# Kernel tuning notes

Hardware: AMD Instinct MI355X
Metric: run time of the kernel (lower is better)

Reference implementation:

```python
import jax, jax.numpy as jnp
import numpy as np

E, H, M, IN, T = 4, 64, 64, 32, 32      # e_size, hidden_state, message, in_size, target
HL = (128, 256, 128)                     # NNet hidden layers (priba's NNet default)
N_LAYERS = 3


def setup_inputs() -> dict:
    key = jax.random.key(0)
    ks = iter(jax.random.split(key, 64))
    B, N = 16, 128

    def w(shape, scale=0.1):
        return jax.random.normal(next(ks), shape, dtype=jnp.float32) * scale

    inp = {
        "h_in": jax.random.normal(next(ks), (B, N, IN), dtype=jnp.float32),
        "am": jax.random.normal(next(ks), (B, N, N, E), dtype=jnp.float32),
        "g_size": jax.random.randint(next(ks), (B,), 0, N),
    }
    # EdgeNetwork NNet: E -> 128 -> 256 -> 128 -> M*H
    dims_e = (E,) + HL + (M * H,)
    for i in range(4):
        inp[f"We{i}"] = w((dims_e[i], dims_e[i + 1]))
        inp[f"be{i}"] = w((dims_e[i + 1],))
    # GRU (torch nn.GRU, one layer, one step): input M, hidden H
    inp["Wih"] = w((3 * H, M)); inp["Whh"] = w((3 * H, H))
    inp["bih"] = w((3 * H,)); inp["bhh"] = w((3 * H,))
    # Readout NNets: i on [h_T, h_0] (H+IN -> T), j on h_T (H -> T)
    dims_i = (H + IN,) + HL + (T,)
    dims_j = (H,) + HL + (T,)
    for i in range(4):
        inp[f"Wi{i}"] = w((dims_i[i], dims_i[i + 1])); inp[f"bi{i}"] = w((dims_i[i + 1],))
        inp[f"Wj{i}"] = w((dims_j[i], dims_j[i + 1])); inp[f"bj{i}"] = w((dims_j[i + 1],))
    return inp


def _mlp(x, Ws, bs):
    for Wk, bk in zip(Ws[:-1], bs[:-1]):
        x = jax.nn.relu(x @ Wk + bk)
    return x @ Ws[-1] + bs[-1]


def reference(h_in, am, g_size,
              We0, be0, We1, be1, We2, be2, We3, be3,
              Wih, Whh, bih, bhh,
              Wi0, bi0, Wi1, bi1, Wi2, bi2, Wi3, bi3,
              Wj0, bj0, Wj1, bj1, Wj2, bj2, Wj3, bj3):
    B, N, _ = h_in.shape
    h = jnp.pad(h_in, ((0, 0), (0, 0), (0, H - IN)))            # pad to hidden size
    mask = (jnp.arange(N)[None, :] < g_size[:, None]).astype(h.dtype)[:, :, None]  # [B,N,1]

    # Edge-network hidden features; final linear layer is fused into the
    # message contraction to avoid materializing per-edge [M,H] matrices.
    f = am                                                       # [B,N,N,E]
    for Wk, bk in ((We0, be0), (We1, be1), (We2, be2)):
        f = jax.nn.relu(f @ Wk + bk)                             # [B,N,N,128]
    W3 = We3.reshape(HL[-1], M, H)                               # [128,M,H]
    b3 = be3.reshape(M, H)

    for _ in range(N_LAYERS):                                    # weight-tied GGNN steps
        # m[b,v,o] = sum_w (A(e_bvw) @ h_bw)[o], A = reshape(f @ We3 + be3)
        t = jnp.einsum('bvwk,bwi->bvki', f, h)                   # [B,N,128,H]
        msg = jnp.einsum('bvki,koi->bvo', t, W3)
        msg = msg + jnp.einsum('oi,bi->bo', b3, h.sum(1))[:, None, :]
        # single-step torch GRU update
        gi = msg @ Wih.T + bih
        gh = h @ Whh.T + bhh
        r = jax.nn.sigmoid(gi[..., :H] + gh[..., :H])
        z = jax.nn.sigmoid(gi[..., H:2 * H] + gh[..., H:2 * H])
        n = jnp.tanh(gi[..., 2 * H:] + r * gh[..., 2 * H:])
        h = (1.0 - z) * n + z * h
        h = h * mask

    # GGNN readout: sum_v mask * sigmoid(i([h_T, h_0])) * j(h_T), then log_softmax
    gate = jax.nn.sigmoid(_mlp(jnp.concatenate([h, h_in], -1),
                               (Wi0, Wi1, Wi2, Wi3), (bi0, bi1, bi2, bi3)))
    val = _mlp(h, (Wj0, Wj1, Wj2, Wj3), (bj0, bj1, bj2, bj3))
    res = (mask * gate * val).sum(1)                             # [B,T]
    return jax.nn.log_softmax(res, axis=1)
```

## Files before the change

kernel.cpp:

```cpp
#include <hip/hip_runtime.h>
#include <math.h>

#define B   16
#define N   128
#define E   4
#define H   64
#define M   64
#define IN_ 32
#define T   32
#define K1  128
#define K2  256
#define K3  128

typedef _Float16 f16;
typedef f16  f16x8 __attribute__((ext_vector_type(8)));
typedef f16  f16x4 __attribute__((ext_vector_type(4)));
typedef f16  f16x2 __attribute__((ext_vector_type(2)));
typedef float f32x4 __attribute__((ext_vector_type(4)));

#define MFMA16(a, b, c) __builtin_amdgcn_mfma_f32_16x16x32_f16(a, b, c, 0, 0, 0)

#define OFF_W1T   0
#define OFF_W2T   32768
#define OFF_WE3H  65536
#define OFF_RI0   589824
#define OFF_RI1   602112
#define OFF_RI2   634880
#define OFF_RI3   667648
#define OFF_RJ0   671744
#define OFF_RJ1   679936
#define OFF_RJ2   712704
#define OFF_RJ3   745472
#define WPACK_SZ  749568

union SmemU {
    struct { float xl[64][4]; f16 y1[64][136]; f16 y2[64][264]; } e;
    union {
        struct { f16 Al[128][72]; f16 Bl[128][72]; } in;
        f16 Ol[128][136];
    } pg;
    struct { float prt[8][64]; float hsum[64]; float bias[64]; } bi;
};

__global__ __launch_bounds__(256) void prep_kernel(
    const float* __restrict__ h_in,
    const float* __restrict__ We1, const float* __restrict__ We2,
    const float* __restrict__ We3,
    const float* __restrict__ Wi0, const float* __restrict__ Wi1,
    const float* __restrict__ Wi2, const float* __restrict__ Wi3,
    const float* __restrict__ Wj0, const float* __restrict__ Wj1,
    const float* __restrict__ Wj2, const float* __restrict__ Wj3,
    float* __restrict__ h, f16* __restrict__ h16, f16* __restrict__ hin16,
    f16* __restrict__ wp) {
    int idx = blockIdx.x * 256 + threadIdx.x;
    if (idx < B * N * H) {
        int i  = idx & (H - 1);
        int bn = idx >> 6;
        float v = (i < IN_) ? h_in[bn * IN_ + i] : 0.f;
        h[idx] = v;
        h16[idx] = (f16)v;
        if (i < IN_) hin16[bn * IN_ + i] = (f16)v;
    }
    if (idx >= WPACK_SZ) return;
    if (idx < OFF_W2T) {
        int j = idx >> 7, k = idx & 127;
        wp[idx] = (f16)We1[k * 256 + j];
    } else if (idx < OFF_WE3H) {
        int t = idx - OFF_W2T;
        int j = t >> 8, k = t & 255;
        wp[idx] = (f16)We2[k * 128 + j];
    } else if (idx < OFF_RI0) {
        wp[idx] = (f16)We3[idx - OFF_WE3H];
    } else if (idx < OFF_RI1) {
        int t = idx - OFF_RI0;
        int n = t / 96, c = t % 96;
        wp[idx] = (f16)Wi0[c * 128 + n];
    } else if (idx < OFF_RI2) {
        int t = idx - OFF_RI1;
        int n = t >> 7, k = t & 127;
        wp[idx] = (f16)Wi1[k * 256 + n];
    } else if (idx < OFF_RI3) {
        int t = idx - OFF_RI2;
        int n = t >> 8, k = t & 255;
        wp[idx] = (f16)Wi2[k * 128 + n];
    } else if (idx < OFF_RJ0) {
        int t = idx - OFF_RI3;
        int n = t >> 7, k = t & 127;
        wp[idx] = (f16)Wi3[k * 32 + n];
    } else if (idx < OFF_RJ1) {
        int t = idx - OFF_RJ0;
        int n = t >> 6, c = t & 63;
        wp[idx] = (f16)Wj0[c * 128 + n];
    } else if (idx < OFF_RJ2) {
        int t = idx - OFF_RJ1;
        int n = t >> 7, k = t & 127;
        wp[idx] = (f16)Wj1[k * 256 + n];
    } else if (idx < OFF_RJ3) {
        int t = idx - OFF_RJ2;
        int n = t >> 8, k = t & 255;
        wp[idx] = (f16)Wj2[k * 128 + n];
    } else {
        int t = idx - OFF_RJ3;
        int n = t >> 7, k = t & 127;
        wp[idx] = (f16)Wj3[k * 32 + n];
    }
}


__device__ void edge_body(SmemU& su, int tid, int tile,
                          const float* __restrict__ am,
                          const float* __restrict__ We0,
                          const float* __restrict__ be0,
                          const f16* __restrict__ W1t,
                          const float* __restrict__ be1,
                          const f16* __restrict__ W2t,
                          const float* __restrict__ be2,
                          f16* __restrict__ f) {
    int lane = tid & 63, wv = tid >> 6;
    long long g0 = (long long)tile * 64;

    if (tid < 256) ((float*)su.e.xl)[tid] = am[g0 * 4 + tid];
    __syncthreads();

    {
        int j0 = (tid & 63) * 2, e0 = (tid >> 6) * 8;
        float w00 = We0[j0],       w01 = We0[j0 + 1];
        float w10 = We0[128 + j0], w11 = We0[128 + j0 + 1];
        float w20 = We0[256 + j0], w21 = We0[256 + j0 + 1];
        float w30 = We0[384 + j0], w31 = We0[384 + j0 + 1];
        float b0 = be0[j0], b1 = be0[j0 + 1];
        #pragma unroll 4
        for (int e = e0; e < e0 + 8; ++e) {
            float x0 = su.e.xl[e][0], x1 = su.e.xl[e][1];
            float x2 = su.e.xl[e][2], x3 = su.e.xl[e][3];
            float v0 = b0 + x0 * w00 + x1 * w10 + x2 * w20 + x3 * w30;
            float v1 = b1 + x0 * w01 + x1 * w11 + x2 * w21 + x3 * w31;
            f16x2 p;
            p[0] = (f16)fmaxf(v0, 0.f);
            p[1] = (f16)fmaxf(v1, 0.f);
            *(f16x2*)&su.e.y1[e][j0] = p;
        }
    }
    __syncthreads();

    int m = lane & 15, q = lane >> 4;

    {
        f32x4 acc[2][4];
        #pragma unroll
        for (int ct = 0; ct < 2; ++ct)
            #pragma unroll
            for (int rt = 0; rt < 4; ++rt) acc[ct][rt] = (f32x4){0.f, 0.f, 0.f, 0.f};
        #pragma unroll
        for (int s = 0; s < 4; ++s) {
            int k0 = s * 32 + q * 8;
            f16x8 afr[4], bfr[2];
            #pragma unroll
            for (int rt = 0; rt < 4; ++rt)
                afr[rt] = *(const f16x8*)&su.e.y1[rt * 16 + m][k0];
            #pragma unroll
            for (int ct = 0; ct < 2; ++ct) {
                int n = (wv * 2 + ct) * 16 + m;
                bfr[ct] = *(const f16x8*)(W1t + n * 128 + k0);
            }
            #pragma unroll
            for (int ct = 0; ct < 2; ++ct)
                #pragma unroll
                for (int rt = 0; rt < 4; ++rt)
                    acc[ct][rt] = MFMA16(bfr[ct], afr[rt], acc[ct][rt]);
        }
        #pragma unroll
        for (int ct = 0; ct < 2; ++ct) {
            int n0 = (wv * 2 + ct) * 16 + q * 4;
            f32x4 bb = *(const f32x4*)&be1[n0];
            #pragma unroll
            for (int rt = 0; rt < 4; ++rt) {
                int e = rt * 16 + m;
                f16x4 pk;
                #pragma unroll
                for (int r = 0; r < 4; ++r)
                    pk[r] = (f16)fmaxf(acc[ct][rt][r] + bb[r], 0.f);
                *(f16x4*)&su.e.y2[e][n0] = pk;
            }
        }
    }
    __syncthreads();

    {
        f32x4 acc[4];
        #pragma unroll
        for (int rt = 0; rt < 4; ++rt) acc[rt] = (f32x4){0.f, 0.f, 0.f, 0.f};
        int n = wv * 16 + m;
        #pragma unroll
        for (int s = 0; s < 8; ++s) {
            int k0 = s * 32 + q * 8;
            f16x8 bfr = *(const f16x8*)(W2t + n * 256 + k0);
            #pragma unroll
            for (int rt = 0; rt < 4; ++rt) {
                f16x8 afr = *(const f16x8*)&su.e.y2[rt * 16 + m][k0];
                acc[rt] = MFMA16(bfr, afr, acc[rt]);
            }
        }
        int n0 = wv * 16 + q * 4;
        f32x4 bb = *(const f32x4*)&be2[n0];
        #pragma unroll
        for (int rt = 0; rt < 4; ++rt) {
            int e = rt * 16 + m;
            f16x4 pk;
            #pragma unroll
            for (int r = 0; r < 4; ++r)
                pk[r] = (f16)fmaxf(acc[rt][r] + bb[r], 0.f);
            *(f16x4*)&su.e.y1[e][n0] = pk;
        }
    }
    __syncthreads();

    #pragma unroll
    for (int j = 0; j < 2; ++j) {
        int c = tid + j * 512;
        int e = c >> 4, pp = c & 15;
        *(uint4*)(f + (g0 + e) * 128 + pp * 8) = *(const uint4*)&su.e.y1[e][pp * 8];
    }
}

__device__ void pgemm_body(SmemU& su, int tid, int ob, int nt,
                           const f16* __restrict__ h16,
                           const f16* __restrict__ We3h,
                           f16* __restrict__ P2) {
    int lane = tid & 63, wv = tid >> 6;

    #pragma unroll
    for (int j = 0; j < 2; ++j) {
        int c = tid + j * 512;
        int row = c >> 3, pp = c & 7;
        *(uint4*)&su.pg.in.Al[row][pp * 8] =
            *(const uint4*)(h16 + (size_t)(nt * 128 + row) * 64 + pp * 8);
    }
    #pragma unroll
    for (int j = 0; j < 2; ++j) {
        int c = tid + j * 512;
        int k = c >> 3, pp = c & 7;
        *(uint4*)&su.pg.in.Bl[k][pp * 8] =
            *(const uint4*)(We3h + ((size_t)(k * 64 + ob)) * 64 + pp * 8);
    }
    __syncthreads();

    int m = lane & 15, q = lane >> 4;
    f32x4 acc[8];
    #pragma unroll
    for (int rt = 0; rt < 8; ++rt) acc[rt] = (f32x4){0.f, 0.f, 0.f, 0.f};
    #pragma unroll
    for (int s = 0; s < 2; ++s) {
        int k0 = s * 32 + q * 8;
        f16x8 afr[8];
        #pragma unroll
        for (int rt = 0; rt < 8; ++rt)
            afr[rt] = *(const f16x8*)&su.pg.in.Al[rt * 16 + m][k0];
        f16x8 bfr = *(const f16x8*)&su.pg.in.Bl[wv * 16 + m][k0];
        #pragma unroll
        for (int rt = 0; rt < 8; ++rt)
            acc[rt] = MFMA16(bfr, afr[rt], acc[rt]);
    }
    __syncthreads();
    {
        int c0 = wv * 16 + q * 4;
        #pragma unroll
        for (int rt = 0; rt < 8; ++rt) {
            int v = rt * 16 + m;
            f16x4 pk;
            #pragma unroll
            for (int r = 0; r < 4; ++r) pk[r] = (f16)acc[rt][r];
            *(f16x4*)&su.pg.Ol[v][c0] = pk;
        }
    }
    __syncthreads();
    #pragma unroll
    for (int j = 0; j < 4; ++j) {
        int c = tid + j * 512;
        int row = c >> 4, pp = c & 15;
        *(uint4*)(P2 + ((size_t)(nt * 128 + row) * 64 + ob) * 128 + pp * 8) =
            *(const uint4*)&su.pg.Ol[row][pp * 8];
    }
}

__device__ void bias_body(SmemU& su, int tid, int b,
                          const float* __restrict__ h,
                          const float* __restrict__ be3,
                          float* __restrict__ biasb) {
    int i = tid & 63, wq = tid >> 6;
    float s = 0.f;
    for (int w = wq; w < N; w += 8) s += h[((size_t)(b * N + w)) * H + i];
    su.bi.prt[wq][i] = s;
    __syncthreads();
    if (tid < 64) {
        float t = 0.f;
        #pragma unroll
        for (int p = 0; p < 8; ++p) t += su.bi.prt[p][tid];
        su.bi.hsum[tid] = t;
    }
    __syncthreads();
    if (tid < 64) {
        float sb = 0.f;
        #pragma unroll 4
        for (int ii = 0; ii < H; ++ii) sb += be3[tid * H + ii] * su.bi.hsum[ii];
        biasb[b * 64 + tid] = sb;
    }
}

__global__ __launch_bounds__(512, 6) void mega0_kernel(
    const float* __restrict__ am,
    const float* __restrict__ We0, const float* __restrict__ be0,
    const float* __restrict__ be1, const float* __restrict__ be2,
    const float* __restrict__ be3,
    const f16* __restrict__ wp,
    const float* __restrict__ h, const f16* __restrict__ h16,
    f16* __restrict__ f, f16* __restrict__ P2, float* __restrict__ biasb) {
    __shared__ SmemU su;
    int tid = threadIdx.x;
    int bid = blockIdx.x;
    if (bid < 4096) {
        edge_body(su, tid, bid, am, We0, be0, wp + OFF_W1T, be1, wp + OFF_W2T,
                  be2, f);
    } else if (bid < 5120) {
        int t = bid - 4096;
        pgemm_body(su, tid, t & 63, t >> 6, h16, wp + OFF_WE3H, P2);
    } else {
        bias_body(su, tid, bid - 5120, h, be3, biasb);
    }
}

__global__ __launch_bounds__(512, 6) void pg_bias_kernel(
    const float* __restrict__ be3, const f16* __restrict__ wp,
    const float* __restrict__ h, const f16* __restrict__ h16,
    f16* __restrict__ P2, float* __restrict__ biasb) {
    __shared__ SmemU su;
    int tid = threadIdx.x;
    int bid = blockIdx.x;
    if (bid < 1024) {
        pgemm_body(su, tid, bid & 63, bid >> 6, h16, wp + OFF_WE3H, P2);
    } else {
        bias_body(su, tid, bid - 1024, h, be3, biasb);
    }
}

__global__ __launch_bounds__(256, 2) void msg_mfma(
    const f16* __restrict__ f, const f16* __restrict__ P2,
    float* __restrict__ part) {
    __shared__ f16 Al[128][136];
    __shared__ f16 Bl[64][136];
    int tid = threadIdx.x, lane = tid & 63, wv = tid >> 6;
    int ws = blockIdx.x;
    int b  = blockIdx.y;
    int m = lane & 15, q = lane >> 4;

    f32x4 acc[2][4];
    #pragma unroll
    for (int rt = 0; rt < 2; ++rt)
        #pragma unroll
        for (int ct = 0; ct < 4; ++ct) acc[rt][ct] = (f32x4){0.f, 0.f, 0.f, 0.f};

    for (int wi = 0; wi < 4; ++wi) {
        int w = ws * 4 + wi;
        #pragma unroll
        for (int j = 0; j < 8; ++j) {
            int c = tid + j * 256;
            int v = c >> 4, pp = c & 15;
            *(uint4*)&Al[v][pp * 8] =
                *(const uint4*)(f + (((size_t)(b * 128 + v) * 128 + w) * 128) + pp * 8);
        }
        #pragma unroll
        for (int j = 0; j < 4; ++j) {
            int c = tid + j * 256;
            int o = c >> 4, pp = c & 15;
            *(uint4*)&Bl[o][pp * 8] =
                *(const uint4*)(P2 + (((size_t)(b * 128 + w) * 64 + o) * 128) + pp * 8);
        }
        __syncthreads();
        #pragma unroll
        for (int s = 0; s < 4; ++s) {
            int k0 = s * 32 + q * 8;
            f16x8 afr[2], bfr[4];
            #pragma unroll
            for (int rt = 0; rt < 2; ++rt)
                afr[rt] = *(const f16x8*)&Al[(wv * 2 + rt) * 16 + m][k0];
            #pragma unroll
            for (int ct = 0; ct < 4; ++ct)
                bfr[ct] = *(const f16x8*)&Bl[ct * 16 + m][k0];
            #pragma unroll
            for (int rt = 0; rt < 2; ++rt)
                #pragma unroll
                for (int ct = 0; ct < 4; ++ct)
                    acc[rt][ct] = MFMA16(afr[rt], bfr[ct], acc[rt][ct]);
        }
        __syncthreads();
    }
    float* pp = part + (size_t)ws * (2048 * 64);
    #pragma unroll
    for (int rt = 0; rt < 2; ++rt)
        #pragma unroll
        for (int ct = 0; ct < 4; ++ct) {
            int o = ct * 16 + m;
            #pragma unroll
            for (int r = 0; r < 4; ++r) {
                int v = (wv * 2 + rt) * 16 + q * 4 + r;
                pp[(size_t)(b * 128 + v) * 64 + o] = acc[rt][ct][r];
            }
        }
}

__global__ __launch_bounds__(192) void gru_kernel(
    const float* __restrict__ biasb, const float* __restrict__ part,
    float* __restrict__ h, f16* __restrict__ h16,
    const float* __restrict__ Wih, const float* __restrict__ Whh,
    const float* __restrict__ bih, const float* __restrict__ bhh,
    const int* __restrict__ g_size) {
    __shared__ float m_lds[M];
    __shared__ float h_lds[H];
    __shared__ float gi[3 * H], gh[3 * H];
    int tid = threadIdx.x;
    int bv  = blockIdx.x;
    int b = bv >> 7, v = bv & 127;

    if (tid < M) {
        float s = biasb[b * 64 + tid];
        #pragma unroll 8
        for (int sp = 0; sp < 32; ++sp)
            s += part[(size_t)sp * (2048 * 64) + bv * 64 + tid];
        m_lds[tid] = s;
    } else if (tid < M + H) {
        h_lds[tid - M] = h[bv * H + (tid - M)];
    }
    __syncthreads();

    {
        float si = bih[tid], sh = bhh[tid];
        const float* wi = Wih + tid * M;
        const float* wh = Whh + tid * H;
        #pragma unroll 4
        for (int k = 0; k < M; ++k) si += wi[k] * m_lds[k];
        #pragma unroll 4
        for (int k = 0; k < H; ++k) sh += wh[k] * h_lds[k];
        gi[tid] = si;
        gh[tid] = sh;
    }
    __syncthreads();
    if (tid < H) {
        float r = 1.f / (1.f + expf(-(gi[tid] + gh[tid])));
        float z = 1.f / (1.f + expf(-(gi[H + tid] + gh[H + tid])));
        float n = tanhf(gi[2 * H + tid] + r * gh[2 * H + tid]);
        float hv = (1.f - z) * n + z * h_lds[tid];
        float maskf = (v < g_size[b]) ? 1.f : 0.f;
        hv *= maskf;
        h[bv * H + tid] = hv;
        h16[bv * H + tid] = (f16)hv;
    }
}

__global__ __launch_bounds__(256, 4) void readout_mfma(
    const f16* __restrict__ h16, const f16* __restrict__ hin16,
    const int* __restrict__ g_size, const f16* __restrict__ wp,
    const float* __restrict__ bi0, const float* __restrict__ bi1,
    const float* __restrict__ bi2, const float* __restrict__ bi3,
    const float* __restrict__ bj0, const float* __restrict__ bj1,
    const float* __restrict__ bj2, const float* __restrict__ bj3,
    float* __restrict__ contrib) {
    __shared__ f16 Xl[16][104];
    __shared__ f16 A1[16][136];
    __shared__ f16 A2[16][264];
    __shared__ float Gl[16][36];
    const f16* Ri0 = wp + OFF_RI0; const f16* Ri1 = wp + OFF_RI1;
    const f16* Ri2 = wp + OFF_RI2; const f16* Ri3 = wp + OFF_RI3;
    const f16* Rj0 = wp + OFF_RJ0; const f16* Rj1 = wp + OFF_RJ1;
    const f16* Rj2 = wp + OFF_RJ2; const f16* Rj3 = wp + OFF_RJ3;
    int tid = threadIdx.x, lane = tid & 63, wv = tid >> 6;
    int m = lane & 15, q = lane >> 4;
    int r0 = blockIdx.x * 16;

    {
        if (tid < 128) {
            int row = tid >> 3, pp = tid & 7;
            *(uint4*)&Xl[row][pp * 8] =
                *(const uint4*)(h16 + (size_t)(r0 + row) * 64 + pp * 8);
        }
        if (tid < 64) {
            int row2 = tid >> 2, p2 = tid & 3;
            *(uint4*)&Xl[row2][64 + p2 * 8] =
                *(const uint4*)(hin16 + (size_t)(r0 + row2) * 32 + p2 * 8);
        }
    }
    __syncthreads();

    {
        f32x4 acc[2];
        acc[0] = (f32x4){0.f, 0.f, 0.f, 0.f};
        acc[1] = (f32x4){0.f, 0.f, 0.f, 0.f};
        #pragma unroll
        for (int s = 0; s < 3; ++s) {
            int k0 = s * 32 + q * 8;
            f16x8 afr = *(const f16x8*)&Xl[m][k0];
            #pragma unroll
            for (int ct = 0; ct < 2; ++ct) {
                f16x8 bfr = *(const f16x8*)(Ri0 + ((wv * 2 + ct) * 16 + m) * 96 + k0);
                acc[ct] = MFMA16(afr, bfr, acc[ct]);
            }
        }
        #pragma unroll
        for (int ct = 0; ct < 2; ++ct) {
            int n = (wv * 2 + ct) * 16 + m;
            float bb = bi0[n];
            #pragma unroll
            for (int r = 0; r < 4; ++r)
                A1[q * 4 + r][n] = (f16)fmaxf(acc[ct][r] + bb, 0.f);
        }
    }
    __syncthreads();

    {
        f32x4 acc[4];
        #pragma unroll
        for (int ct = 0; ct < 4; ++ct) acc[ct] = (f32x4){0.f, 0.f, 0.f, 0.f};
        #pragma unroll
        for (int s = 0; s < 4; ++s) {
            int k0 = s * 32 + q * 8;
            f16x8 afr = *(const f16x8*)&A1[m][k0];
            #pragma unroll
            for (int ct = 0; ct < 4; ++ct) {
                f16x8 bfr = *(const f16x8*)(Ri1 + ((wv * 4 + ct) * 16 + m) * 128 + k0);
                acc[ct] = MFMA16(afr, bfr, acc[ct]);
            }
        }
        #pragma unroll
        for (int ct = 0; ct < 4; ++ct) {
            int n = (wv * 4 + ct) * 16 + m;
            float bb = bi1[n];
            #pragma unroll
            for (int r = 0; r < 4; ++r)
                A2[q * 4 + r][n] = (f16)fmaxf(acc[ct][r] + bb, 0.f);
        }
    }
    __syncthreads();

    {
        f32x4 acc[2];
        acc[0] = (f32x4){0.f, 0.f, 0.f, 0.f};
        acc[1] = (f32x4){0.f, 0.f, 0.f, 0.f};
        #pragma unroll
        for (int s = 0; s < 8; ++s) {
            int k0 = s * 32 + q * 8;
            f16x8 afr = *(const f16x8*)&A2[m][k0];
            #pragma unroll
            for (int ct = 0; ct < 2; ++ct) {
                f16x8 bfr = *(const f16x8*)(Ri2 + ((wv * 2 + ct) * 16 + m) * 256 + k0);
                acc[ct] = MFMA16(afr, bfr, acc[ct]);
            }
        }
        __syncthreads();
        #pragma unroll
        for (int ct = 0; ct < 2; ++ct) {
            int n = (wv * 2 + ct) * 16 + m;
            float bb = bi2[n];
            #pragma unroll
            for (int r = 0; r < 4; ++r)
                A1[q * 4 + r][n] = (f16)fmaxf(acc[ct][r] + bb, 0.f);
        }
    }
    __syncthreads();

    if (wv < 2) {
        f32x4 acc = (f32x4){0.f, 0.f, 0.f, 0.f};
        int n = wv * 16 + m;
        #pragma unroll
        for (int s = 0; s < 4; ++s) {
            int k0 = s * 32 + q * 8;
            f16x8 bfr = *(const f16x8*)(Ri3 + n * 128 + k0);
            f16x8 afr = *(const f16x8*)&A1[m][k0];
            acc = MFMA16(afr, bfr, acc);
        }
        float bb = bi3[n];
        #pragma unroll
        for (int r = 0; r < 4; ++r)
            Gl[q * 4 + r][n] = 1.f / (1.f + expf(-(acc[r] + bb)));
    }
    __syncthreads();

    {
        f32x4 acc[2];
        acc[0] = (f32x4){0.f, 0.f, 0.f, 0.f};
        acc[1] = (f32x4){0.f, 0.f, 0.f, 0.f};
        #pragma unroll
        for (int s = 0; s < 2; ++s) {
            int k0 = s * 32 + q * 8;
            f16x8 afr = *(const f16x8*)&Xl[m][k0];
            #pragma unroll
            for (int ct = 0; ct < 2; ++ct) {
                f16x8 bfr = *(const f16x8*)(Rj0 + ((wv * 2 + ct) * 16 + m) * 64 + k0);
                acc[ct] = MFMA16(afr, bfr, acc[ct]);
            }
        }
        __syncthreads();
        #pragma unroll
        for (int ct = 0; ct < 2; ++ct) {
            int n = (wv * 2 + ct) * 16 + m;
            float bb = bj0[n];
            #pragma unroll
            for (int r = 0; r < 4; ++r)
                A1[q * 4 + r][n] = (f16)fmaxf(acc[ct][r] + bb, 0.f);
        }
    }
    __syncthreads();

    {
        f32x4 acc[4];
        #pragma unroll
        for (int ct = 0; ct < 4; ++ct) acc[ct] = (f32x4){0.f, 0.f, 0.f, 0.f};
        #pragma unroll
        for (int s = 0; s < 4; ++s) {
            int k0 = s * 32 + q * 8;
            f16x8 afr = *(const f16x8*)&A1[m][k0];
            #pragma unroll
            for (int ct = 0; ct < 4; ++ct) {
                f16x8 bfr = *(const f16x8*)(Rj1 + ((wv * 4 + ct) * 16 + m) * 128 + k0);
                acc[ct] = MFMA16(afr, bfr, acc[ct]);
            }
        }
        #pragma unroll
        for (int ct = 0; ct < 4; ++ct) {
            int n = (wv * 4 + ct) * 16 + m;
            float bb = bj1[n];
            #pragma unroll
            for (int r = 0; r < 4; ++r)
                A2[q * 4 + r][n] = (f16)fmaxf(acc[ct][r] + bb, 0.f);
        }
    }
    __syncthreads();

    {
        f32x4 acc[2];
        acc[0] = (f32x4){0.f, 0.f, 0.f, 0.f};
        acc[1] = (f32x4){0.f, 0.f, 0.f, 0.f};
        #pragma unroll
        for (int s = 0; s < 8; ++s) {
            int k0 = s * 32 + q * 8;
            f16x8 afr = *(const f16x8*)&A2[m][k0];
            #pragma unroll
            for (int ct = 0; ct < 2; ++ct) {
                f16x8 bfr = *(const f16x8*)(Rj2 + ((wv * 2 + ct) * 16 + m) * 256 + k0);
                acc[ct] = MFMA16(afr, bfr, acc[ct]);
            }
        }
        __syncthreads();
        #pragma unroll
        for (int ct = 0; ct < 2; ++ct) {
            int n = (wv * 2 + ct) * 16 + m;
            float bb = bj2[n];
            #pragma unroll
            for (int r = 0; r < 4; ++r)
                A1[q * 4 + r][n] = (f16)fmaxf(acc[ct][r] + bb, 0.f);
        }
    }
    __syncthreads();

    if (wv < 2) {
        f32x4 acc = (f32x4){0.f, 0.f, 0.f, 0.f};
        int n = wv * 16 + m;
        #pragma unroll
        for (int s = 0; s < 4; ++s) {
            int k0 = s * 32 + q * 8;
            f16x8 bfr = *(const f16x8*)(Rj3 + n * 128 + k0);
            f16x8 afr = *(const f16x8*)&A1[m][k0];
            acc = MFMA16(afr, bfr, acc);
        }
        float bb = bj3[n];
        #pragma unroll
        for (int r = 0; r < 4; ++r) {
            int row = q * 4 + r;
            int rg = r0 + row;
            int b = rg >> 7, v = rg & 127;
            float maskf = (v < g_size[b]) ? 1.f : 0.f;
            contrib[(size_t)rg * T + n] = maskf * Gl[row][n] * (acc[r] + bb);
        }
    }
}

__global__ __launch_bounds__(64) void finalize_kernel(const float* __restrict__ contrib,
                                                      float* __restrict__ out) {
    __shared__ float res[T];
    int b = blockIdx.x;
    int o = threadIdx.x;
    if (o < T) {
        float s = 0.f;
        for (int v = 0; v < N; ++v) s += contrib[(b * N + v) * T + o];
        res[o] = s;
    }
    __syncthreads();
    if (o < T) {
        float mx = res[0];
        for (int i = 1; i < T; ++i) mx = fmaxf(mx, res[i]);
        float se = 0.f;
        for (int i = 0; i < T; ++i) se += expf(res[i] - mx);
        out[b * T + o] = res[o] - mx - logf(se);
    }
}

extern "C" void kernel_launch(void* const* d_in, const int* in_sizes, int n_in,
                              void* d_out, int out_size, void* d_ws, size_t ws_size,
                              hipStream_t stream) {
    (void)in_sizes; (void)n_in; (void)out_size; (void)ws_size;
    const float* h_in = (const float*)d_in[0];
    const float* am   = (const float*)d_in[1];
    const int*   g_sz = (const int*)d_in[2];
    const float* We0 = (const float*)d_in[3],  *be0 = (const float*)d_in[4];
    const float* We1 = (const float*)d_in[5],  *be1 = (const float*)d_in[6];
    const float* We2 = (const float*)d_in[7],  *be2 = (const float*)d_in[8];
    const float* We3 = (const float*)d_in[9],  *be3 = (const float*)d_in[10];
    const float* Wih = (const float*)d_in[11], *Whh = (const float*)d_in[12];
    const float* bih = (const float*)d_in[13], *bhh = (const float*)d_in[14];
    const float* Wi0 = (const float*)d_in[15], *bi0 = (const float*)d_in[16];
    const float* Wj0 = (const float*)d_in[17], *bj0 = (const float*)d_in[18];
    const float* Wi1 = (const float*)d_in[19], *bi1 = (const float*)d_in[20];
    const float* Wj1 = (const float*)d_in[21], *bj1 = (const float*)d_in[22];
    const float* Wi2 = (const float*)d_in[23], *bi2 = (const float*)d_in[24];
    const float* Wj2 = (const float*)d_in[25], *bj2 = (const float*)d_in[26];
    const float* Wi3 = (const float*)d_in[27], *bi3 = (const float*)d_in[28];
    const float* Wj3 = (const float*)d_in[29], *bj3 = (const float*)d_in[30];

    float* out = (float*)d_out;

    f16*   f    = (f16*)d_ws;
    f16*   P2   = f + (size_t)33554432;
    float* part = (float*)(P2 + (size_t)16777216);
    float* h    = part + (size_t)4194304;
    float* biasb = h + 131072;
    float* contrib = biasb + 1024;
    f16*   h16  = (f16*)(contrib + 65536);
    f16*   hin16 = h16 + 131072;
    f16*   wp   = hin16 + 65536;

    prep_kernel<<<(WPACK_SZ + 255) / 256, 256, 0, stream>>>(
        h_in, We1, We2, We3, Wi0, Wi1, Wi2, Wi3, Wj0, Wj1, Wj2, Wj3,
        h, h16, hin16, wp);

    mega0_kernel<<<4096 + 1024 + 16, 512, 0, stream>>>(
        am, We0, be0, be1, be2, be3, wp, h, h16, f, P2, biasb);
    msg_mfma<<<dim3(32, 16), 256, 0, stream>>>(f, P2, part);
    gru_kernel<<<B * N, 192, 0, stream>>>(biasb, part, h, h16,
                                          Wih, Whh, bih, bhh, g_sz);

    for (int l = 1; l < 3; ++l) {
        pg_bias_kernel<<<1024 + 16, 512, 0, stream>>>(be3, wp, h, h16, P2, biasb);
        msg_mfma<<<dim3(32, 16), 256, 0, stream>>>(f, P2, part);
        gru_kernel<<<B * N, 192, 0, stream>>>(biasb, part, h, h16,
                                              Wih, Whh, bih, bhh, g_sz);
    }

    readout_mfma<<<128, 256, 0, stream>>>(h16, hin16, g_sz, wp,
                                          bi0, bi1, bi2, bi3,
                                          bj0, bj1, bj2, bj3, contrib);
    finalize_kernel<<<B, 64, 0, stream>>>(contrib, out);
}
```

Measured before the change: 419.7 us.

## Halve block size of edge/pgemm kernels and store split-K partials in fp16

The edge-network and P-GEMM kernels move from 512 to 256 threads per block, and each wave now computes twice as many output tiles (more accumulators, more MFMAs per loaded fragment). This raises operand reuse per wave and cuts barrier participants, at the cost of more registers per thread and lower occupancy. Separately, the split-K message partials written by msg_mfma and read by the GRU kernel are stored as fp16 instead of fp32. That halves that traffic but adds rounding error to the 32-way partial sums.

```diff
diff --git a/kernel.cpp b/kernel.cpp
--- a/kernel.cpp
+++ b/kernel.cpp
@@ -39,7 +39,7 @@
         struct { f16 Al[128][72]; f16 Bl[128][72]; } in;
         f16 Ol[128][136];
     } pg;
-    struct { float prt[8][64]; float hsum[64]; float bias[64]; } bi;
+    struct { float prt[4][64]; float hsum[64]; float bias[64]; } bi;
 };
 
 __global__ __launch_bounds__(256) void prep_kernel(
@@ -119,18 +119,18 @@
     int lane = tid & 63, wv = tid >> 6;
     long long g0 = (long long)tile * 64;
 
-    if (tid < 256) ((float*)su.e.xl)[tid] = am[g0 * 4 + tid];
-    __syncthreads();
-
-    {
-        int j0 = (tid & 63) * 2, e0 = (tid >> 6) * 8;
+    ((float*)su.e.xl)[tid] = am[g0 * 4 + tid];
+    __syncthreads();
+
+    {
+        int j0 = (tid & 63) * 2, e0 = (tid >> 6) * 16;
         float w00 = We0[j0],       w01 = We0[j0 + 1];
         float w10 = We0[128 + j0], w11 = We0[128 + j0 + 1];
         float w20 = We0[256 + j0], w21 = We0[256 + j0 + 1];
         float w30 = We0[384 + j0], w31 = We0[384 + j0 + 1];
         float b0 = be0[j0], b1 = be0[j0 + 1];
         #pragma unroll 4
-        for (int e = e0; e < e0 + 8; ++e) {
+        for (int e = e0; e < e0 + 16; ++e) {
             float x0 = su.e.xl[e][0], x1 = su.e.xl[e][1];
             float x2 = su.e.xl[e][2], x3 = su.e.xl[e][3];
             float v0 = b0 + x0 * w00 + x1 * w10 + x2 * w20 + x3 * w30;
@@ -146,32 +146,32 @@
     int m = lane & 15, q = lane >> 4;
 
     {
-        f32x4 acc[2][4];
-        #pragma unroll
-        for (int ct = 0; ct < 2; ++ct)
+        f32x4 acc[4][4];
+        #pragma unroll
+        for (int ct = 0; ct < 4; ++ct)
             #pragma unroll
             for (int rt = 0; rt < 4; ++rt) acc[ct][rt] = (f32x4){0.f, 0.f, 0.f, 0.f};
         #pragma unroll
         for (int s = 0; s < 4; ++s) {
             int k0 = s * 32 + q * 8;
-            f16x8 afr[4], bfr[2];
+            f16x8 afr[4], bfr[4];
             #pragma unroll
             for (int rt = 0; rt < 4; ++rt)
                 afr[rt] = *(const f16x8*)&su.e.y1[rt * 16 + m][k0];
             #pragma unroll
-            for (int ct = 0; ct < 2; ++ct) {
-                int n = (wv * 2 + ct) * 16 + m;
+            for (int ct = 0; ct < 4; ++ct) {
+                int n = (wv * 4 + ct) * 16 + m;
                 bfr[ct] = *(const f16x8*)(W1t + n * 128 + k0);
             }
             #pragma unroll
-            for (int ct = 0; ct < 2; ++ct)
+            for (int ct = 0; ct < 4; ++ct)
                 #pragma unroll
                 for (int rt = 0; rt < 4; ++rt)
                     acc[ct][rt] = MFMA16(bfr[ct], afr[rt], acc[ct][rt]);
         }
         #pragma unroll
-        for (int ct = 0; ct < 2; ++ct) {
-            int n0 = (wv * 2 + ct) * 16 + q * 4;
+        for (int ct = 0; ct < 4; ++ct) {
+            int n0 = (wv * 4 + ct) * 16 + q * 4;
             f32x4 bb = *(const f32x4*)&be1[n0];
             #pragma unroll
             for (int rt = 0; rt < 4; ++rt) {
@@ -187,37 +187,49 @@
     __syncthreads();
 
     {
-        f32x4 acc[4];
-        #pragma unroll
-        for (int rt = 0; rt < 4; ++rt) acc[rt] = (f32x4){0.f, 0.f, 0.f, 0.f};
-        int n = wv * 16 + m;
+        f32x4 acc[2][4];
+        #pragma unroll
+        for (int ct = 0; ct < 2; ++ct)
+            #pragma unroll
+            for (int rt = 0; rt < 4; ++rt) acc[ct][rt] = (f32x4){0.f, 0.f, 0.f, 0.f};
         #pragma unroll
         for (int s = 0; s < 8; ++s) {
             int k0 = s * 32 + q * 8;
-            f16x8 bfr = *(const f16x8*)(W2t + n * 256 + k0);
+            f16x8 afr[4], bfr[2];
+            #pragma unroll
+            for (int rt = 0; rt < 4; ++rt)
+                afr[rt] = *(const f16x8*)&su.e.y2[rt * 16 + m][k0];
+            #pragma unroll
+            for (int ct = 0; ct < 2; ++ct) {
+                int n = (wv * 2 + ct) * 16 + m;
+                bfr[ct] = *(const f16x8*)(W2t + n * 256 + k0);
+            }
+            #pragma unroll
+            for (int ct = 0; ct < 2; ++ct)
+                #pragma unroll
+                for (int rt = 0; rt < 4; ++rt)
+                    acc[ct][rt] = MFMA16(bfr[ct], afr[rt], acc[ct][rt]);
+        }
+        #pragma unroll
+        for (int ct = 0; ct < 2; ++ct) {
+            int n0 = (wv * 2 + ct) * 16 + q * 4;
+            f32x4 bb = *(const f32x4*)&be2[n0];
             #pragma unroll
             for (int rt = 0; rt < 4; ++rt) {
-                f16x8 afr = *(const f16x8*)&su.e.y2[rt * 16 + m][k0];
-                acc[rt] = MFMA16(bfr, afr, acc[rt]);
-            }
-        }
-        int n0 = wv * 16 + q * 4;
-        f32x4 bb = *(const f32x4*)&be2[n0];
-        #pragma unroll
-        for (int rt = 0; rt < 4; ++rt) {
-            int e = rt * 16 + m;
-            f16x4 pk;
-            #pragma unroll
-            for (int r = 0; r < 4; ++r)
-                pk[r] = (f16)fmaxf(acc[rt][r] + bb[r], 0.f);
-            *(f16x4*)&su.e.y1[e][n0] = pk;
-        }
-    }
-    __syncthreads();
-
-    #pragma unroll
-    for (int j = 0; j < 2; ++j) {
-        int c = tid + j * 512;
+                int e = rt * 16 + m;
+                f16x4 pk;
+                #pragma unroll
+                for (int r = 0; r < 4; ++r)
+                    pk[r] = (f16)fmaxf(acc[ct][rt][r] + bb[r], 0.f);
+                *(f16x4*)&su.e.y1[e][n0] = pk;
+            }
+        }
+    }
+    __syncthreads();
+
+    #pragma unroll
+    for (int j = 0; j < 4; ++j) {
+        int c = tid + j * 256;
         int e = c >> 4, pp = c & 15;
         *(uint4*)(f + (g0 + e) * 128 + pp * 8) = *(const uint4*)&su.e.y1[e][pp * 8];
     }
@@ -230,15 +242,15 @@
     int lane = tid & 63, wv = tid >> 6;
 
     #pragma unroll
-    for (int j = 0; j < 2; ++j) {
-        int c = tid + j * 512;
+    for (int j = 0; j < 4; ++j) {
+        int c = tid + j * 256;
         int row = c >> 3, pp = c & 7;
         *(uint4*)&su.pg.in.Al[row][pp * 8] =
             *(const uint4*)(h16 + (size_t)(nt * 128 + row) * 64 + pp * 8);
     }
     #pragma unroll
-    for (int j = 0; j < 2; ++j) {
-        int c = tid + j * 512;
+    for (int j = 0; j < 4; ++j) {
+        int c = tid + j * 256;
         int k = c >> 3, pp = c & 7;
         *(uint4*)&su.pg.in.Bl[k][pp * 8] =
             *(const uint4*)(We3h + ((size_t)(k * 64 + ob)) * 64 + pp * 8);
@@ -246,37 +258,44 @@
     __syncthreads();
 
     int m = lane & 15, q = lane >> 4;
-    f32x4 acc[8];
-    #pragma unroll
-    for (int rt = 0; rt < 8; ++rt) acc[rt] = (f32x4){0.f, 0.f, 0.f, 0.f};
+    f32x4 acc[2][8];
+    #pragma unroll
+    for (int ct = 0; ct < 2; ++ct)
+        #pragma unroll
+        for (int rt = 0; rt < 8; ++rt) acc[ct][rt] = (f32x4){0.f, 0.f, 0.f, 0.f};
     #pragma unroll
     for (int s = 0; s < 2; ++s) {
         int k0 = s * 32 + q * 8;
-        f16x8 afr[8];
+        f16x8 afr[8], bfr[2];
         #pragma unroll
         for (int rt = 0; rt < 8; ++rt)
             afr[rt] = *(const f16x8*)&su.pg.in.Al[rt * 16 + m][k0];
-        f16x8 bfr = *(const f16x8*)&su.pg.in.Bl[wv * 16 + m][k0];
-        #pragma unroll
-        for (int rt = 0; rt < 8; ++rt)
-            acc[rt] = MFMA16(bfr, afr[rt], acc[rt]);
-    }
-    __syncthreads();
-    {
-        int c0 = wv * 16 + q * 4;
+        #pragma unroll
+        for (int ct = 0; ct < 2; ++ct)
+            bfr[ct] = *(const f16x8*)&su.pg.in.Bl[(wv * 2 + ct) * 16 + m][k0];
+        #pragma unroll
+        for (int ct = 0; ct < 2; ++ct)
+            #pragma unroll
+            for (int rt = 0; rt < 8; ++rt)
+                acc[ct][rt] = MFMA16(bfr[ct], afr[rt], acc[ct][rt]);
+    }
+    __syncthreads();
+    #pragma unroll
+    for (int ct = 0; ct < 2; ++ct) {
+        int c0 = (wv * 2 + ct) * 16 + q * 4;
         #pragma unroll
         for (int rt = 0; rt < 8; ++rt) {
             int v = rt * 16 + m;
             f16x4 pk;
             #pragma unroll
-            for (int r = 0; r < 4; ++r) pk[r] = (f16)acc[rt][r];
+            for (int r = 0; r < 4; ++r) pk[r] = (f16)acc[ct][rt][r];
             *(f16x4*)&su.pg.Ol[v][c0] = pk;
         }
     }
     __syncthreads();
     #pragma unroll
-    for (int j = 0; j < 4; ++j) {
-        int c = tid + j * 512;
+    for (int j = 0; j < 8; ++j) {
+        int c = tid + j * 256;
         int row = c >> 4, pp = c & 15;
         *(uint4*)(P2 + ((size_t)(nt * 128 + row) * 64 + ob) * 128 + pp * 8) =
             *(const uint4*)&su.pg.Ol[row][pp * 8];
@@ -289,15 +308,12 @@
                           float* __restrict__ biasb) {
     int i = tid & 63, wq = tid >> 6;
     float s = 0.f;
-    for (int w = wq; w < N; w += 8) s += h[((size_t)(b * N + w)) * H + i];
+    for (int w = wq; w < N; w += 4) s += h[((size_t)(b * N + w)) * H + i];
     su.bi.prt[wq][i] = s;
     __syncthreads();
-    if (tid < 64) {
-        float t = 0.f;
-        #pragma unroll
-        for (int p = 0; p < 8; ++p) t += su.bi.prt[p][tid];
-        su.bi.hsum[tid] = t;
-    }
+    if (tid < 64)
+        su.bi.hsum[tid] = su.bi.prt[0][tid] + su.bi.prt[1][tid]
+                        + su.bi.prt[2][tid] + su.bi.prt[3][tid];
     __syncthreads();
     if (tid < 64) {
         float sb = 0.f;
@@ -307,7 +323,7 @@
     }
 }
 
-__global__ __launch_bounds__(512, 6) void mega0_kernel(
+__global__ __launch_bounds__(256, 3) void mega0_kernel(
     const float* __restrict__ am,
     const float* __restrict__ We0, const float* __restrict__ be0,
     const float* __restrict__ be1, const float* __restrict__ be2,
@@ -329,7 +345,7 @@
     }
 }
 
-__global__ __launch_bounds__(512, 6) void pg_bias_kernel(
+__global__ __launch_bounds__(256, 3) void pg_bias_kernel(
     const float* __restrict__ be3, const f16* __restrict__ wp,
     const float* __restrict__ h, const f16* __restrict__ h16,
     f16* __restrict__ P2, float* __restrict__ biasb) {
@@ -345,7 +361,7 @@
 
 __global__ __launch_bounds__(256, 2) void msg_mfma(
     const f16* __restrict__ f, const f16* __restrict__ P2,
-    float* __restrict__ part) {
+    f16* __restrict__ part) {
     __shared__ f16 Al[128][136];
     __shared__ f16 Bl[64][136];
     int tid = threadIdx.x, lane = tid & 63, wv = tid >> 6;
@@ -394,7 +410,7 @@
         }
         __syncthreads();
     }
-    float* pp = part + (size_t)ws * (2048 * 64);
+    f16* pp = part + (size_t)ws * (2048 * 64);
     #pragma unroll
     for (int rt = 0; rt < 2; ++rt)
         #pragma unroll
@@ -403,13 +419,13 @@
             #pragma unroll
             for (int r = 0; r < 4; ++r) {
                 int v = (wv * 2 + rt) * 16 + q * 4 + r;
-                pp[(size_t)(b * 128 + v) * 64 + o] = acc[rt][ct][r];
+                pp[(size_t)(b * 128 + v) * 64 + o] = (f16)acc[rt][ct][r];
             }
         }
 }
 
 __global__ __launch_bounds__(192) void gru_kernel(
-    const float* __restrict__ biasb, const float* __restrict__ part,
+    const float* __restrict__ biasb, const f16* __restrict__ part,
     float* __restrict__ h, f16* __restrict__ h16,
     const float* __restrict__ Wih, const float* __restrict__ Whh,
     const float* __restrict__ bih, const float* __restrict__ bhh,
@@ -425,7 +441,7 @@
         float s = biasb[b * 64 + tid];
         #pragma unroll 8
         for (int sp = 0; sp < 32; ++sp)
-            s += part[(size_t)sp * (2048 * 64) + bv * 64 + tid];
+            s += (float)part[(size_t)sp * (2048 * 64) + bv * 64 + tid];
         m_lds[tid] = s;
     } else if (tid < M + H) {
         h_lds[tid - M] = h[bv * H + (tid - M)];
@@ -728,8 +744,8 @@
 
     f16*   f    = (f16*)d_ws;
     f16*   P2   = f + (size_t)33554432;
-    float* part = (float*)(P2 + (size_t)16777216);
-    float* h    = part + (size_t)4194304;
+    f16*   part = P2 + (size_t)16777216;
+    float* h    = (float*)(part + (size_t)4194304);
     float* biasb = h + 131072;
     float* contrib = biasb + 1024;
     f16*   h16  = (f16*)(contrib + 65536);
@@ -740,14 +756,14 @@
         h_in, We1, We2, We3, Wi0, Wi1, Wi2, Wi3, Wj0, Wj1, Wj2, Wj3,
         h, h16, hin16, wp);
 
-    mega0_kernel<<<4096 + 1024 + 16, 512, 0, stream>>>(
+    mega0_kernel<<<4096 + 1024 + 16, 256, 0, stream>>>(
         am, We0, be0, be1, be2, be3, wp, h, h16, f, P2, biasb);
     msg_mfma<<<dim3(32, 16), 256, 0, stream>>>(f, P2, part);
     gru_kernel<<<B * N, 192, 0, stream>>>(biasb, part, h, h16,
                                           Wih, Whh, bih, bhh, g_sz);
 
     for (int l = 1; l < 3; ++l) {
-        pg_bias_kernel<<<1024 + 16, 512, 0, stream>>>(be3, wp, h, h16, P2, biasb);
+        pg_bias_kernel<<<1024 + 16, 256, 0, stream>>>(be3, wp, h, h16, P2, biasb);
         msg_mfma<<<dim3(32, 16), 256, 0, stream>>>(f, P2, part);
         gru_kernel<<<B * N, 192, 0, stream>>>(biasb, part, h, h16,
                                               Wih, Whh, bih, bhh, g_sz);
```

After: 387.7 us. -7.6%, faster.
